# Kernel tuning notes

Measured on AMD Instinct MI355X. Metric: run time of the kernel, lower is better.

## Reference

```python
import jax, jax.numpy as jnp
import numpy as np

IN_F = 135; D = 512; K = 10; DCT_N = 34; IN_N = 120; OUT_N = 24
VL = K + OUT_N          # 34, window length
VN = IN_N - K - OUT_N + 1  # 87, number of windows
NSTAGE = 2
BN_SCALE = 1.0 / np.sqrt(1.0 + 1e-5)  # eval-mode BN with default running stats (mean 0, var 1)


def get_dct_matrix(N):
    dct_m = np.eye(N)
    for k in range(N):
        for i in range(N):
            w = np.sqrt(2.0 / N)
            if k == 0:
                w = np.sqrt(1.0 / N)
            dct_m[k, i] = w * np.cos(np.pi * (i + 0.5) * k / N)
    idct_m = np.linalg.inv(dct_m)
    return dct_m, idct_m

_DCT_NP, _IDCT_NP = get_dct_matrix(VL)
DCT = jnp.asarray(_DCT_NP[:DCT_N], dtype=jnp.float32)        # [34,34] (dct_n == vl)
IDCT = jnp.asarray(_IDCT_NP[:, :DCT_N], dtype=jnp.float32)   # [34,34]

WIN_IDX = np.arange(VL)[None, :] + np.arange(VN)[:, None]    # [87,34]
PAD_IDX = np.concatenate([np.arange(IN_N - K, IN_N), np.full(OUT_N, IN_N - 1)])  # last 10 frames + last frame repeated


def conv1d(x, w):
    return jax.lax.conv_general_dilated(x, w, (1,), 'VALID',
                                        dimension_numbers=('NCH', 'OIH', 'NCH'))


def gconv(x, att, w, b):
    # GraphConvolution: att @ (x @ w) + b ; x: [b,n,f_in]
    return jnp.einsum('nm,bmf->bnf', att, x @ w) + b


def bn_eval(y, g, b):
    bs, n, f = y.shape
    v = y.reshape(bs, n * f)
    v = g * (v * BN_SCALE) + b
    return v.reshape(bs, n, f)


def setup_inputs() -> dict:
    key = jax.random.key(0)
    ks = jax.random.split(key, 20)
    s = 0.05  # small init scale so tanh/att stay in sane range
    return {
        'poses':    jax.random.normal(ks[0], (256, 144, 135), jnp.float32),
        'qw1':      jax.random.normal(ks[1], (512, 135, 6)) * s,
        'qw2':      jax.random.normal(ks[2], (512, 512, 5)) * s,
        'kw1':      jax.random.normal(ks[3], (512, 135, 6)) * s,
        'kw2':      jax.random.normal(ks[4], (512, 512, 5)) * s,
        'gc1_att':  jax.random.normal(ks[5], (135, 135)) * s,
        'gc1_w':    jax.random.normal(ks[6], (68, 512)) * s,
        'gc1_b':    jax.random.normal(ks[7], (512,)) * s,
        'bn1_g':    jnp.ones((69120,), jnp.float32),
        'bn1_b':    jnp.zeros((69120,), jnp.float32),
        'gcb_att':  jax.random.normal(ks[8], (4, 135, 135)) * s,
        'gcb_w':    jax.random.normal(ks[9], (4, 512, 512)) * s,
        'gcb_b':    jax.random.normal(ks[10], (4, 512)) * s,
        'gcb_g':    jnp.ones((4, 69120), jnp.float32),
        'gcb_beta': jnp.zeros((4, 69120), jnp.float32),
        'gc7_att':  jax.random.normal(ks[11], (135, 135)) * s,
        'gc7_w':    jax.random.normal(ks[12], (512, 68)) * s,
        'gc7_b':    jax.random.normal(ks[13], (68,)) * s,
    }


def reference(poses, qw1, qw2, kw1, kw2,
              gc1_att, gc1_w, gc1_b, bn1_g, bn1_b,
              gcb_att, gcb_w, gcb_b, gcb_g, gcb_beta,
              gc7_att, gc7_w, gc7_b):
    src = poses[:, :IN_N]                      # [b,120,135]
    bs = src.shape[0]
    src_t = jnp.transpose(src, (0, 2, 1))      # [b,135,120]
    key_in = src_t[:, :, :IN_N - OUT_N] / 1000.0   # [b,135,96]
    qry_in = src_t[:, :, -K:] / 1000.0             # [b,135,10]

    key_f = jax.nn.relu(conv1d(jax.nn.relu(conv1d(key_in, kw1)), kw2))  # [b,512,87]
    qry_f = jax.nn.relu(conv1d(jax.nn.relu(conv1d(qry_in, qw1)), qw2))  # [b,512,1]

    # non-softmax attention: matmul + eps-normalize
    score = jnp.einsum('bdq,bdk->bqk', qry_f, key_f) + 1e-15   # [b,1,87]
    att = score / jnp.sum(score, axis=2, keepdims=True)

    # overlapping windows -> DCT of each window
    windows = src[:, WIN_IDX]                                   # [b,87,34,135]
    val = jnp.einsum('kt,bvtf->bvfk', DCT, windows).reshape(bs, VN, IN_F * DCT_N)
    dct_att = jnp.einsum('bqv,bvz->bqz', att, val)[:, 0].reshape(bs, IN_F, DCT_N)

    input_gcn = src[:, PAD_IDX]                                 # [b,34,135]
    dct_in = jnp.einsum('kt,btf->bfk', DCT, input_gcn)          # [b,135,34]
    x = jnp.concatenate([dct_in, dct_att], axis=-1)             # [b,135,68]

    # GCN (eval mode: dropout = identity, BN uses running stats)
    y = jnp.tanh(bn_eval(gconv(x, gc1_att, gc1_w, gc1_b), bn1_g, bn1_b))
    for i in range(NSTAGE):
        res = y
        h = jnp.tanh(bn_eval(gconv(y, gcb_att[2 * i], gcb_w[2 * i], gcb_b[2 * i]),
                             gcb_g[2 * i], gcb_beta[2 * i]))
        h = jnp.tanh(bn_eval(gconv(h, gcb_att[2 * i + 1], gcb_w[2 * i + 1], gcb_b[2 * i + 1]),
                             gcb_g[2 * i + 1], gcb_beta[2 * i + 1]))
        y = h + res
    y = gconv(y, gc7_att, gc7_w, gc7_b) + x                     # [b,135,68]

    out = jnp.einsum('tk,bfk->btf', IDCT, y[:, :, :DCT_N])      # [b,34,135]
    preds = out[:, -OUT_N:, :]                                  # [b,24,135]
    return preds
```

## Files before the change

kernel.cpp:

```cpp
#include <hip/hip_runtime.h>
#include <math.h>

#define POSE_ROWS 144
#define NF 135
#define DD 512
#define KQ 10
#define DCTN 34
#define INN 120
#define OUTN 24
#define VN 87
#define BATCH 256
#define RP 34816
#define NODEP 136
#define BN_SCALE 0.9999950000374997f

typedef __attribute__((ext_vector_type(8))) short short8;
typedef __attribute__((ext_vector_type(4))) float floatx4;

static __device__ __forceinline__ ushort f2bf(float f) {
    unsigned u = __builtin_bit_cast(unsigned, f);
    u = (u + 0x7FFFu + ((u >> 16) & 1u)) >> 16;
    return (ushort)u;
}
static __device__ __forceinline__ float bf2f(ushort s) {
    return __builtin_bit_cast(float, (unsigned)s << 16);
}
static __device__ __forceinline__ float tanh_fast(float x) {
    float ax = __builtin_fabsf(x);
    float e = __builtin_amdgcn_exp2f(ax * -2.885390081777927f);
    float t = (1.f - e) * __builtin_amdgcn_rcpf(1.f + e);
    return __builtin_copysignf(t, x);
}

#define GLOAD_LDS(gp, lp) __builtin_amdgcn_global_load_lds( \
    (const __attribute__((address_space(1))) unsigned int*)(const void*)(gp), \
    (__attribute__((address_space(3))) unsigned int*)(void*)(lp), 16, 0, 0)

#define PB_POSES 19584
#define PB_K1B   22912
#define PB_K2B   33152
#define PB_WT1   33408
#define PB_WTB   37504
#define PB_WT7   37640
#define PB_A1    37742
#define PB_AB    38147
#define PB_A7    38249
#define PB_BN    39609
#define PB_Z     39610
#define PB_DCT   39615

__global__ __launch_bounds__(256) void prep_all(
    const float* __restrict__ poses, ushort* __restrict__ pb16,
    const float* __restrict__ kw1, const float* __restrict__ qw1,
    ushort* __restrict__ Wt1k, ushort* __restrict__ Wt1q,
    const float* __restrict__ kw2, const float* __restrict__ qw2,
    ushort* __restrict__ Wt2k, ushort* __restrict__ Wt2q,
    const float* __restrict__ gc1_w, ushort* __restrict__ WT1,
    const float* __restrict__ gcb_w, ushort* __restrict__ WTb,
    const float* __restrict__ gc7_w, ushort* __restrict__ WT7,
    const float* __restrict__ gc1_att, ushort* __restrict__ A16_1,
    const float* __restrict__ gcb_att, ushort* __restrict__ A16_B,
    const float* __restrict__ gc7_att, ushort* __restrict__ A16_7,
    const float* __restrict__ bn1_g, const float* __restrict__ bn1_b,
    const float* __restrict__ gcb_g, const float* __restrict__ gcb_beta,
    float* __restrict__ bnT, float* __restrict__ zpadf, float* __restrict__ dct)
{
    const int blk = blockIdx.x;
    const int tid = threadIdx.x;
    if (blk < PB_POSES) {
        int idx = blk * 256 + tid;
        int i = idx % NODEP;
        int row = (idx / NODEP) % POSE_ROWS;
        int b = idx / (NODEP * POSE_ROWS);
        float v = (i < NF) ? poses[((long long)b * POSE_ROWS + row) * NF + i] * 1e-3f : 0.f;
        pb16[idx] = f2bf(v);
    } else if (blk < PB_K1B) {
        int wi = blk - PB_POSES;
        const float* src = (wi < 1664) ? kw1 : qw1;
        ushort* dst = (wi < 1664) ? Wt1k : Wt1q;
        int idx = (wi % 1664) * 256 + tid;
        int n = idx / 832, k = idx % 832;
        int h = k / 136, i = k % 136;
        float v = (i < 135 && h < 6) ? src[((long long)n * 135 + i) * 6 + h] : 0.f;
        dst[idx] = f2bf(v);
    } else if (blk < PB_K2B) {
        int wi = blk - PB_K1B;
        const float* src = (wi < 5120) ? kw2 : qw2;
        ushort* dst = (wi < 5120) ? Wt2k : Wt2q;
        int idx = (wi % 5120) * 256 + tid;
        int n = idx / 2560, k = idx % 2560;
        int h = k / 512, i = k % 512;
        dst[idx] = f2bf(src[((long long)n * 512 + i) * 5 + h]);
    } else if (blk < PB_WT1) {
        int idx = (blk - PB_K2B) * 256 + tid;
        int n = idx / 128, k = idx % 128;
        WT1[idx] = f2bf((k < 68) ? gc1_w[(long long)k * 512 + n] : 0.f);
    } else if (blk < PB_WTB) {
        int g = (blk - PB_WT1) * 256 + tid;
        int L = g >> 18, idx = g & 262143;
        int n = idx / 512, k = idx % 512;
        WTb[g] = f2bf(gcb_w[(long long)L * 262144 + (long long)k * 512 + n]);
    } else if (blk < PB_WT7) {
        int idx = (blk - PB_WTB) * 256 + tid;
        int n = idx / 512, k = idx % 512;
        WT7[idx] = f2bf(gc7_w[(long long)k * 68 + n]);
    } else if (blk < PB_A1) {
        int idx = (blk - PB_WT7) * 256 + tid;
        if (idx < 135 * 192) {
            int r = idx / 192, c = idx % 192;
            A16_1[idx] = f2bf(c < 135 ? gc1_att[r * 135 + c] : 0.f);
        }
    } else if (blk < PB_AB) {
        int idx = (blk - PB_A1) * 256 + tid;
        int r = idx / 192, c = idx % 192;
        A16_B[idx] = f2bf(c < 135 ? gcb_att[r * 135 + c] : 0.f);
    } else if (blk < PB_A7) {
        int idx = (blk - PB_AB) * 256 + tid;
        if (idx < 135 * 192) {
            int r = idx / 192, c = idx % 192;
            A16_7[idx] = f2bf(c < 135 ? gc7_att[r * 135 + c] : 0.f);
        }
    } else if (blk < PB_BN) {
        int g = (blk - PB_A7) * 256 + tid;
        int p = g / 69632, idx = g % 69632;
        int node = idx % 136, m = idx / 136;
        const float* gs = (p == 0) ? bn1_g : (gcb_g + (p - 1) * 69120);
        const float* bs = (p == 0) ? bn1_b : (gcb_beta + (p - 1) * 69120);
        float* gt = bnT + (long long)p * 139264;
        float* bt = gt + 69632;
        gt[idx] = (node < 135) ? gs[node * 512 + m] : 0.f;
        bt[idx] = (node < 135) ? bs[node * 512 + m] : 0.f;
    } else if (blk < PB_Z) {
        if (tid < 128) zpadf[tid] = 0.f;
    } else {
        int idx = (blk - PB_Z) * 256 + tid;
        if (idx < DCTN * DCTN) {
            int k = idx / DCTN, i = idx % DCTN;
            double w = (k == 0) ? sqrt(1.0 / DCTN) : sqrt(2.0 / DCTN);
            dct[idx] = (float)(w * cos(3.14159265358979323846 * (i + 0.5) * k / (double)DCTN));
        }
    }
}

template<int BM, int BN>
__global__ __launch_bounds__(256) void gemm2(
    const ushort* __restrict__ A, const ushort* __restrict__ Bt,
    const ushort* __restrict__ zpad,
    int M, int N, int K,
    int mode, int CNT, int Pc,
    int rpbA, long long sAw, long long sAr, long long sAbz,
    long long sBr, long long sBbz,
    float* __restrict__ C, ushort* __restrict__ C16,
    long long sCbz, long long sCm, long long sCn,
    int do_relu, const float* __restrict__ bias, int bias_mode,
    const float* __restrict__ bnTg, const float* __restrict__ bnTb,
    int do_tanh, const ushort* __restrict__ resid16, const float* __restrict__ resid32)
{
    constexpr int SM = BM / 32, SN = BN / 32;
    constexpr int RA = BM / 32, RB = BN / 32;
    __shared__ ushort As[BM * 64];
    __shared__ ushort Bs[BN * 64];

    int mb, nb;
    if (mode == 0) { mb = blockIdx.y; nb = blockIdx.x; }
    else {
        int gx = blockIdx.x;
        int x = gx & 7, s = gx >> 3;
        if (mode == 1) { mb = s % CNT; nb = x * Pc + s / CNT; }
        else           { nb = s % CNT; mb = x * Pc + s / CNT; }
    }
    const int m0 = mb * BM, n0 = nb * BN;
    if (m0 >= M || n0 >= N) return;

    const int tid = threadIdx.x;
    const int lane = tid & 63, w = tid >> 6;
    const int bz = blockIdx.z;
    const int wm = (w >> 1) * (BM / 2), wn = (w & 1) * (BN / 2);
    const int chunk = (lane & 7) ^ ((lane >> 3) & 7);

    const ushort* pA[RA]; int stA[RA];
    #pragma unroll
    for (int j = 0; j < RA; j++) {
        int m = m0 + j * 32 + w * 8 + (lane >> 3);
        bool v = m < M;
        long long off = v ? ((long long)(m / rpbA) * sAw + (long long)(m % rpbA) * sAr
                            + (long long)bz * sAbz) : 0;
        pA[j] = v ? (A + off + chunk * 8) : (zpad + chunk * 8);
        stA[j] = v ? 64 : 0;
    }
    const ushort* pB[RB]; int stB[RB];
    #pragma unroll
    for (int j = 0; j < RB; j++) {
        int n = n0 + j * 32 + w * 8 + (lane >> 3);
        bool v = n < N;
        long long off = v ? ((long long)n * sBr + (long long)bz * sBbz) : 0;
        pB[j] = v ? (Bt + off + chunk * 8) : (zpad + chunk * 8);
        stB[j] = v ? 64 : 0;
    }

    floatx4 acc[SM][SN];
    #pragma unroll
    for (int i = 0; i < SM; i++)
        #pragma unroll
        for (int j = 0; j < SN; j++)
            acc[i][j] = (floatx4){0.f, 0.f, 0.f, 0.f};

    for (int k0 = 0; k0 < K; k0 += 64) {
        #pragma unroll
        for (int j = 0; j < RA; j++)
            GLOAD_LDS(pA[j], &As[(j * 32 + w * 8) * 64]);
        #pragma unroll
        for (int j = 0; j < RB; j++)
            GLOAD_LDS(pB[j], &Bs[(j * 32 + w * 8) * 64]);
        __syncthreads();

        #pragma unroll
        for (int kk = 0; kk < 2; kk++) {
            short8 af[SM], bf[SN];
            #pragma unroll
            for (int sm = 0; sm < SM; sm++) {
                int lr = wm + sm * 16 + (lane & 15);
                int slot = ((lane >> 4) + kk * 4) ^ (lr & 7);
                af[sm] = *(const short8*)&As[lr * 64 + slot * 8];
            }
            #pragma unroll
            for (int sn = 0; sn < SN; sn++) {
                int lr = wn + sn * 16 + (lane & 15);
                int slot = ((lane >> 4) + kk * 4) ^ (lr & 7);
                bf[sn] = *(const short8*)&Bs[lr * 64 + slot * 8];
            }
            #pragma unroll
            for (int sm = 0; sm < SM; sm++)
                #pragma unroll
                for (int sn = 0; sn < SN; sn++)
                    acc[sm][sn] = __builtin_amdgcn_mfma_f32_16x16x32_bf16(af[sm], bf[sn], acc[sm][sn], 0, 0, 0);
        }
        __syncthreads();

        #pragma unroll
        for (int j = 0; j < RA; j++) pA[j] += stA[j];
        #pragma unroll
        for (int j = 0; j < RB; j++) pB[j] += stB[j];
    }

    const int lc = lane & 15;
    const int lr4 = (lane >> 4) << 2;
    #pragma unroll
    for (int sm = 0; sm < SM; sm++) {
        #pragma unroll
        for (int sn = 0; sn < SN; sn++) {
            int n = n0 + wn + sn * 16 + lc;
            if (n >= N) continue;
            int node = n % 136;
            int mbv = m0 + wm + sm * 16 + lr4;
            float vv[4];
            #pragma unroll
            for (int r = 0; r < 4; r++) {
                int m = mbv + r;
                float v = acc[sm][sn][r];
                if (do_relu) v = fmaxf(v, 0.f);
                if (bias) v += (bias_mode == 1) ? bias[m < M ? m : 0] : bias[n];
                if (bnTg) {
                    long long gi = (long long)(m < M ? m : 0) * 136 + node;
                    v = bnTg[gi] * (v * BN_SCALE) + bnTb[gi];
                }
                if (do_tanh) v = tanh_fast(v);
                long long addr = (long long)bz * sCbz + (long long)m * sCm + (long long)n * sCn;
                if (m < M) {
                    if (resid16) v += bf2f(resid16[addr]);
                    else if (resid32) v += resid32[addr];
                    if (C) C[addr] = v;
                    if (C16 && sCm != 1) C16[addr] = f2bf(v);
                }
                vv[r] = v;
            }
            if (C16 && sCm == 1 && mbv + 3 < M) {
                ushort4 pk;
                pk.x = f2bf(vv[0]); pk.y = f2bf(vv[1]); pk.z = f2bf(vv[2]); pk.w = f2bf(vv[3]);
                *(ushort4*)&C16[(long long)bz * sCbz + mbv + (long long)n * sCn] = pk;
            }
        }
    }
}

__global__ __launch_bounds__(512) void fused_layer(
    const ushort* __restrict__ Yin,
    const ushort* __restrict__ Att,
    const ushort* __restrict__ Wt,
    const ushort* __restrict__ zpad,
    const float* __restrict__ bias,
    const float* __restrict__ bnTg, const float* __restrict__ bnTb,
    const ushort* __restrict__ resid16,
    ushort* __restrict__ Yout)
{
    extern __shared__ ushort zs[];
    const int b = blockIdx.x;
    const int tid = threadIdx.x;
    const int lane = tid & 63, w = tid >> 6;
    const int ln = lane & 15;
    const int lk8 = (lane >> 4) * 8;
    const int lr4 = (lane >> 4) << 2;
    const long long ybase = (long long)b * 136;
    const int cp = w * 64;

    {
        const ushort* pb[9];
        #pragma unroll
        for (int nt = 0; nt < 9; nt++) {
            int n = nt * 16 + ln;
            pb[nt] = (n < 135) ? (Att + (long long)n * 192 + lk8) : (zpad + lk8);
        }
        const ushort* pa[4];
        #pragma unroll
        for (int sm = 0; sm < 4; sm++) {
            int c = cp + sm * 16 + ln;
            pa[sm] = Yin + (long long)c * RP + ybase + lk8;
        }
        floatx4 acc[4][9];
        #pragma unroll
        for (int i = 0; i < 4; i++)
            #pragma unroll
            for (int j = 0; j < 9; j++)
                acc[i][j] = (floatx4){0.f, 0.f, 0.f, 0.f};

        #pragma unroll
        for (int ks = 0; ks < 5; ks++) {
            const int ko = ks * 32;
            short8 af[4];
            #pragma unroll
            for (int sm = 0; sm < 4; sm++)
                af[sm] = *(const short8*)(pa[sm] + ko);
            #pragma unroll
            for (int nt = 0; nt < 9; nt++) {
                short8 bfv = *(const short8*)(pb[nt] + ko);
                #pragma unroll
                for (int sm = 0; sm < 4; sm++)
                    acc[sm][nt] = __builtin_amdgcn_mfma_f32_16x16x32_bf16(af[sm], bfv, acc[sm][nt], 0, 0, 0);
            }
        }
        #pragma unroll
        for (int sm = 0; sm < 4; sm++) {
            #pragma unroll
            for (int nt = 0; nt < 9; nt++) {
                int n = nt * 16 + ln;
                if (n >= 136) continue;
                int c = cp + sm * 16 + lr4;
                ushort4 pk;
                pk.x = f2bf(acc[sm][nt][0]);
                pk.y = f2bf(acc[sm][nt][1]);
                pk.z = f2bf(acc[sm][nt][2]);
                pk.w = f2bf(acc[sm][nt][3]);
                int chs = (c >> 3) ^ (n & 7);
                *(ushort4*)&zs[n * 512 + chs * 8 + (c & 7)] = pk;
            }
        }
    }
    __syncthreads();

    {
        const ushort* pw[4];
        #pragma unroll
        for (int sm = 0; sm < 4; sm++)
            pw[sm] = Wt + (long long)(cp + sm * 16 + ln) * 512 + lk8;
        int zrow[9], zx[9];
        #pragma unroll
        for (int nt = 0; nt < 9; nt++) {
            int n = nt * 16 + ln;
            int nn = (n < 136) ? n : 0;
            zrow[nt] = nn * 512;
            zx[nt] = nn & 7;
        }
        floatx4 acc[4][9];
        #pragma unroll
        for (int i = 0; i < 4; i++)
            #pragma unroll
            for (int j = 0; j < 9; j++)
                acc[i][j] = (floatx4){0.f, 0.f, 0.f, 0.f};

        #pragma unroll
        for (int ks = 0; ks < 16; ks++) {
            const int ko = ks * 32;
            const int kchunk = ks * 4 + (lane >> 4);
            short8 af[4];
            #pragma unroll
            for (int sm = 0; sm < 4; sm++)
                af[sm] = *(const short8*)(pw[sm] + ko);
            #pragma unroll
            for (int nt = 0; nt < 9; nt++) {
                short8 bfv = *(const short8*)&zs[zrow[nt] + (kchunk ^ zx[nt]) * 8];
                #pragma unroll
                for (int sm = 0; sm < 4; sm++)
                    acc[sm][nt] = __builtin_amdgcn_mfma_f32_16x16x32_bf16(af[sm], bfv, acc[sm][nt], 0, 0, 0);
            }
        }
        #pragma unroll
        for (int sm = 0; sm < 4; sm++) {
            #pragma unroll
            for (int nt = 0; nt < 9; nt++) {
                int n = nt * 16 + ln;
                if (n >= 136) continue;
                int c2 = cp + sm * 16 + lr4;
                #pragma unroll
                for (int r = 0; r < 4; r++) {
                    int m = c2 + r;
                    float v = acc[sm][nt][r];
                    v += bias[m];
                    long long gi = (long long)m * 136 + n;
                    v = bnTg[gi] * (v * BN_SCALE) + bnTb[gi];
                    v = tanh_fast(v);
                    long long addr = (long long)m * RP + ybase + n;
                    if (resid16) v += bf2f(resid16[addr]);
                    Yout[addr] = f2bf(v);
                }
            }
        }
    }
}

__global__ __launch_bounds__(256) void att_k(const float* __restrict__ kf, const float* __restrict__ qf,
                                             float* __restrict__ att) {
    int b = blockIdx.x;
    int tid = threadIdx.x;
    int lane = tid & 63, w = tid >> 6;
    __shared__ float s[96];
    __shared__ float ssum;
    const float* qb = qf + b * DD + lane * 8;
    float4 q0 = *(const float4*)qb;
    float4 q1 = *(const float4*)(qb + 4);
    const float* kb = kf + (long long)b * VN * DD;
    for (int v = w; v < VN; v += 4) {
        const float* kr = kb + v * DD + lane * 8;
        float4 k0 = *(const float4*)kr;
        float4 k1 = *(const float4*)(kr + 4);
        float p = q0.x * k0.x + q0.y * k0.y + q0.z * k0.z + q0.w * k0.w
                + q1.x * k1.x + q1.y * k1.y + q1.z * k1.z + q1.w * k1.w;
        #pragma unroll
        for (int off = 32; off; off >>= 1) p += __shfl_xor(p, off);
        if (lane == 0) s[v] = p + 1e-15f;
    }
    __syncthreads();
    if (tid < 64) {
        float p2 = (tid < VN ? s[tid] : 0.f) + ((tid + 64) < VN ? s[tid + 64] : 0.f);
        #pragma unroll
        for (int off = 32; off; off >>= 1) p2 += __shfl_xor(p2, off);
        if (tid == 0) ssum = p2;
    }
    __syncthreads();
    float inv = 1.f / ssum;
    for (int v = tid; v < VN; v += 256) att[b * VN + v] = s[v] * inv;
}

__global__ void weighted_k(const float* __restrict__ poses, const float* __restrict__ att,
                           float* __restrict__ w34) {
    int t = blockIdx.x;
    int b = blockIdx.y;
    int f = threadIdx.x;
    if (f >= NF) return;
    const float* pb = poses + (long long)b * POSE_ROWS * NF + t * NF + f;
    const float* ab = att + b * VN;
    float acc = 0.f;
    for (int v = 0; v < VN; v++) acc += ab[v] * pb[v * NF];
    w34[(long long)b * DCTN * NF + t * NF + f] = acc;
}

__global__ void build_x(const float* __restrict__ poses, const float* __restrict__ w34,
                        const float* __restrict__ dctm, float* __restrict__ x32,
                        ushort* __restrict__ xT16) {
    int idx = blockIdx.x * 256 + threadIdx.x;
    if (idx >= BATCH * NF * 68) return;
    int kk = idx % 68;
    int f = (idx / 68) % NF;
    int b = idx / (68 * NF);
    float acc = 0.f;
    if (kk < DCTN) {
        const float* pb = poses + (long long)b * POSE_ROWS * NF;
        #pragma unroll
        for (int t = 0; t < DCTN; t++) {
            int row = (t < KQ) ? (INN - KQ + t) : (INN - 1);
            acc += dctm[kk * DCTN + t] * pb[row * NF + f];
        }
    } else {
        int k2 = kk - DCTN;
        const float* wb = w34 + (long long)b * DCTN * NF + f;
        #pragma unroll
        for (int t = 0; t < DCTN; t++) acc += dctm[k2 * DCTN + t] * wb[t * NF];
    }
    long long R = (long long)b * NODEP + f;
    x32[R * 68 + kk] = acc;
    xT16[(long long)kk * RP + R] = f2bf(acc);
}

__global__ void idct_out(const float* __restrict__ h32, const float* __restrict__ dctm,
                         float* __restrict__ out) {
    int idx = blockIdx.x * 256 + threadIdx.x;
    if (idx >= BATCH * OUTN * NF) return;
    int f = idx % NF;
    int t = (idx / NF) % OUTN;
    int b = idx / (NF * OUTN);
    const float* yr = h32 + ((long long)b * NODEP + f) * 68;
    float acc = 0.f;
    #pragma unroll
    for (int k = 0; k < DCTN; k++) acc += dctm[k * DCTN + (KQ + t)] * yr[k];
    out[idx] = acc;
}

extern "C" void kernel_launch(void* const* d_in, const int* in_sizes, int n_in,
                              void* d_out, int out_size, void* d_ws, size_t ws_size,
                              hipStream_t stream) {
    const float* poses   = (const float*)d_in[0];
    const float* qw1     = (const float*)d_in[1];
    const float* qw2     = (const float*)d_in[2];
    const float* kw1     = (const float*)d_in[3];
    const float* kw2     = (const float*)d_in[4];
    const float* gc1_att = (const float*)d_in[5];
    const float* gc1_w   = (const float*)d_in[6];
    const float* gc1_b   = (const float*)d_in[7];
    const float* bn1_g   = (const float*)d_in[8];
    const float* bn1_b   = (const float*)d_in[9];
    const float* gcb_att = (const float*)d_in[10];
    const float* gcb_w   = (const float*)d_in[11];
    const float* gcb_b   = (const float*)d_in[12];
    const float* gcb_g   = (const float*)d_in[13];
    const float* gcb_beta= (const float*)d_in[14];
    const float* gc7_att = (const float*)d_in[15];
    const float* gc7_w   = (const float*)d_in[16];
    const float* gc7_b   = (const float*)d_in[17];
    float* out = (float*)d_out;
    float* w = (float*)d_ws;

    float* dct   = w;
    float* att   = w + 1280;
    float* w34   = w + 23808;
    float* x32   = w + 1198848;
    float* h32   = w + 3566336;
    float* qf    = w + 5933824;
    ushort* su   = (ushort*)(w + 6064896);
    ushort* WT1    = su;
    ushort* WTb    = su + 65536;
    ushort* WT7    = su + 1114112;
    ushort* A16_1  = su + 1148928;
    ushort* A16_B  = su + 1174848;
    ushort* A16_7  = su + 1278528;
    float* bnT   = w + 6717120;
    float* kf    = w + 7413440;
    ushort* R2   = (ushort*)(w + 18816704);
    ushort* yT16  = R2;
    ushort* r1k16 = R2;
    ushort* r1q16 = R2 + 11927552;
    ushort* R3   = (ushort*)(w + 27729600);
    ushort* hT16  = R3;
    ushort* pb16  = R3;
    ushort* Wt1k  = R3 + 5013504;
    ushort* Wt1q  = R3 + 5439488;
    ushort* Wt2k  = R3 + 5865472;
    ushort* Wt2q  = R3 + 7176192;
    ushort* R4   = (ushort*)(w + 36642496);
    ushort* zN16  = R4;
    ushort* xT16  = R4;
    ushort* z116  = R4 + 2367488;
    float* zpadf = w + 45555392;
    const ushort* zpad = (const ushort*)zpadf;

    const int INF_RPB = 1 << 30;

    static int lds_set = 0;
    if (!lds_set) {
        hipFuncSetAttribute((const void*)fused_layer,
                            hipFuncAttributeMaxDynamicSharedMemorySize, 139264);
        lds_set = 1;
    }

    prep_all<<<PB_DCT, 256, 0, stream>>>(
        poses, pb16, kw1, qw1, Wt1k, Wt1q, kw2, qw2, Wt2k, Wt2q,
        gc1_w, WT1, gcb_w, WTb, gc7_w, WT7,
        gc1_att, A16_1, gcb_att, A16_B, gc7_att, A16_7,
        bn1_g, bn1_b, gcb_g, gcb_beta, bnT, zpadf, dct);

    gemm2<128,64><<<dim3(1472, 1, 1), 256, 0, stream>>>(pb16, Wt1k, zpad, 23296, 512, 832,
        2, 8, 23, 91, 19584LL, 136LL, 0LL, 832LL, 0LL,
        (float*)nullptr, r1k16, 0LL, 512LL, 1LL, 1, nullptr, 0, nullptr, nullptr, 0, nullptr, nullptr);
    gemm2<128,128><<<dim3(4, 10, 1), 256, 0, stream>>>(pb16 + 110*136, Wt1q, zpad, 1280, 512, 832,
        0, 0, 0, 5, 19584LL, 136LL, 0LL, 832LL, 0LL,
        (float*)nullptr, r1q16, 0LL, 512LL, 1LL, 1, nullptr, 0, nullptr, nullptr, 0, nullptr, nullptr);
    gemm2<128,64><<<dim3(1408, 1, 1), 256, 0, stream>>>(r1k16, Wt2k, zpad, 22272, 512, 2560,
        2, 8, 22, 87, 46592LL, 512LL, 0LL, 2560LL, 0LL,
        kf, (ushort*)nullptr, 0LL, 512LL, 1LL, 1, nullptr, 0, nullptr, nullptr, 0, nullptr, nullptr);
    gemm2<64,64><<<dim3(8, 4, 1), 256, 0, stream>>>(r1q16, Wt2q, zpad, 256, 512, 2560,
        0, 0, 0, INF_RPB, 0LL, 2560LL, 0LL, 2560LL, 0LL,
        qf, (ushort*)nullptr, 0LL, 512LL, 1LL, 1, nullptr, 0, nullptr, nullptr, 0, nullptr, nullptr);

    att_k<<<BATCH, 256, 0, stream>>>(kf, qf, att);
    weighted_k<<<dim3(DCTN, BATCH), 192, 0, stream>>>(poses, att, w34);
    build_x<<<(BATCH * NF * 68 + 255) / 256, 256, 0, stream>>>(poses, w34, dct, x32, xT16);

    gemm2<64,64><<<dim3(3, 2, BATCH), 256, 0, stream>>>(xT16, A16_1, zpad, 68, 135, 192,
        0, 0, 0, INF_RPB, 0LL, (long long)RP, 136LL, 192LL, 0LL,
        (float*)nullptr, z116, 10880LL, 1LL, 80LL, 0, nullptr, 0, nullptr, nullptr, 0, nullptr, nullptr);
    gemm2<128,64><<<dim3(2176, 1, 1), 256, 0, stream>>>(WT1, z116, zpad, 512, RP, 128,
        1, 4, 68, INF_RPB, 0LL, 128LL, 0LL, 80LL, 0LL,
        (float*)nullptr, yT16, 0LL, (long long)RP, 1LL, 0, gc1_b, 1, bnT, bnT + 69632, 1, nullptr, nullptr);

    for (int L = 0; L < 4; L++) {
        const ushort* min = (L & 1) ? hT16 : yT16;
        ushort* mout = (L & 1) ? yT16 : hT16;
        fused_layer<<<dim3(BATCH, 1, 1), 512, 139264, stream>>>(
            min, A16_B + L * 25920, WTb + L * 262144, zpad,
            gcb_b + L * 512, bnT + (1 + L) * 139264, bnT + (1 + L) * 139264 + 69632,
            (L & 1) ? yT16 : (const ushort*)nullptr, mout);
    }

    gemm2<64,64><<<dim3(3, 8, BATCH), 256, 0, stream>>>(yT16, A16_7, zpad, 512, 135, 192,
        0, 0, 0, INF_RPB, 0LL, (long long)RP, 136LL, 192LL, 0LL,
        (float*)nullptr, zN16, 69632LL, 1LL, 512LL, 0, nullptr, 0, nullptr, nullptr, 0, nullptr, nullptr);
    gemm2<64,64><<<dim3(1088, 1, 1), 256, 0, stream>>>(zN16, WT7, zpad, RP, 68, 512,
        2, 2, 68, INF_RPB, 0LL, 512LL, 0LL, 512LL, 0LL,
        h32, (ushort*)nullptr, 0LL, 68LL, 1LL, 0, gc7_b, 2, nullptr, nullptr, 0, nullptr, x32);

    idct_out<<<(BATCH * OUTN * NF + 255) / 256, 256, 0, stream>>>(h32, dct, out);
}
```

Measured before the change: 895.7 us.

## Store GCN activations batch-major so each sample's features are contiguous

Changes the activation layout yT16/hT16 from channel-major with batch interleaved (stride RP per channel) to batch-major (BSTRIDE per sample, 136 per channel). The gc1 epilogue gets a bmaj addressing mode, and fused_layer and the gc7 att GEMM are updated to index the new layout. The intent is for each fused_layer block to read and write one contiguous 139 KB slab instead of 512 strided rows spread across the whole tensor, which should improve cache and DRAM locality. In exchange, the gc1 epilogue's stores are now scattered by n/136, which may coalesce less well.

```diff
diff --git a/kernel.cpp b/kernel.cpp
--- a/kernel.cpp
+++ b/kernel.cpp
@@ -12,6 +12,7 @@
 #define BATCH 256
 #define RP 34816
 #define NODEP 136
+#define BSTRIDE 69632
 #define BN_SCALE 0.9999950000374997f
 
 typedef __attribute__((ext_vector_type(8))) short short8;
@@ -154,7 +155,8 @@
     long long sCbz, long long sCm, long long sCn,
     int do_relu, const float* __restrict__ bias, int bias_mode,
     const float* __restrict__ bnTg, const float* __restrict__ bnTb,
-    int do_tanh, const ushort* __restrict__ resid16, const float* __restrict__ resid32)
+    int do_tanh, const ushort* __restrict__ resid16, const float* __restrict__ resid32,
+    int bmaj)
 {
     constexpr int SM = BM / 32, SN = BN / 32;
     constexpr int RA = BM / 32, RB = BN / 32;
@@ -265,7 +267,9 @@
                     v = bnTg[gi] * (v * BN_SCALE) + bnTb[gi];
                 }
                 if (do_tanh) v = tanh_fast(v);
-                long long addr = (long long)bz * sCbz + (long long)m * sCm + (long long)n * sCn;
+                long long addr = bmaj
+                    ? (long long)(n / 136) * BSTRIDE + (long long)m * 136 + node
+                    : (long long)bz * sCbz + (long long)m * sCm + (long long)n * sCn;
                 if (m < M) {
                     if (resid16) v += bf2f(resid16[addr]);
                     else if (resid32) v += resid32[addr];
@@ -300,7 +304,7 @@
     const int ln = lane & 15;
     const int lk8 = (lane >> 4) * 8;
     const int lr4 = (lane >> 4) << 2;
-    const long long ybase = (long long)b * 136;
+    const long long ybase = (long long)b * BSTRIDE;
     const int cp = w * 64;
 
     {
@@ -314,7 +318,7 @@
         #pragma unroll
         for (int sm = 0; sm < 4; sm++) {
             int c = cp + sm * 16 + ln;
-            pa[sm] = Yin + (long long)c * RP + ybase + lk8;
+            pa[sm] = Yin + ybase + (long long)c * 136 + lk8;
         }
         floatx4 acc[4][9];
         #pragma unroll
@@ -408,7 +412,7 @@
                     long long gi = (long long)m * 136 + n;
                     v = bnTg[gi] * (v * BN_SCALE) + bnTb[gi];
                     v = tanh_fast(v);
-                    long long addr = (long long)m * RP + ybase + n;
+                    long long addr = ybase + (long long)m * 136 + n;
                     if (resid16) v += bf2f(resid16[addr]);
                     Yout[addr] = f2bf(v);
                 }
@@ -578,16 +582,16 @@
 
     gemm2<128,64><<<dim3(1472, 1, 1), 256, 0, stream>>>(pb16, Wt1k, zpad, 23296, 512, 832,
         2, 8, 23, 91, 19584LL, 136LL, 0LL, 832LL, 0LL,
-        (float*)nullptr, r1k16, 0LL, 512LL, 1LL, 1, nullptr, 0, nullptr, nullptr, 0, nullptr, nullptr);
+        (float*)nullptr, r1k16, 0LL, 512LL, 1LL, 1, nullptr, 0, nullptr, nullptr, 0, nullptr, nullptr, 0);
     gemm2<128,128><<<dim3(4, 10, 1), 256, 0, stream>>>(pb16 + 110*136, Wt1q, zpad, 1280, 512, 832,
         0, 0, 0, 5, 19584LL, 136LL, 0LL, 832LL, 0LL,
-        (float*)nullptr, r1q16, 0LL, 512LL, 1LL, 1, nullptr, 0, nullptr, nullptr, 0, nullptr, nullptr);
+        (float*)nullptr, r1q16, 0LL, 512LL, 1LL, 1, nullptr, 0, nullptr, nullptr, 0, nullptr, nullptr, 0);
     gemm2<128,64><<<dim3(1408, 1, 1), 256, 0, stream>>>(r1k16, Wt2k, zpad, 22272, 512, 2560,
         2, 8, 22, 87, 46592LL, 512LL, 0LL, 2560LL, 0LL,
-        kf, (ushort*)nullptr, 0LL, 512LL, 1LL, 1, nullptr, 0, nullptr, nullptr, 0, nullptr, nullptr);
+        kf, (ushort*)nullptr, 0LL, 512LL, 1LL, 1, nullptr, 0, nullptr, nullptr, 0, nullptr, nullptr, 0);
     gemm2<64,64><<<dim3(8, 4, 1), 256, 0, stream>>>(r1q16, Wt2q, zpad, 256, 512, 2560,
         0, 0, 0, INF_RPB, 0LL, 2560LL, 0LL, 2560LL, 0LL,
-        qf, (ushort*)nullptr, 0LL, 512LL, 1LL, 1, nullptr, 0, nullptr, nullptr, 0, nullptr, nullptr);
+        qf, (ushort*)nullptr, 0LL, 512LL, 1LL, 1, nullptr, 0, nullptr, nullptr, 0, nullptr, nullptr, 0);
 
     att_k<<<BATCH, 256, 0, stream>>>(kf, qf, att);
     weighted_k<<<dim3(DCTN, BATCH), 192, 0, stream>>>(poses, att, w34);
@@ -595,10 +599,10 @@
 
     gemm2<64,64><<<dim3(3, 2, BATCH), 256, 0, stream>>>(xT16, A16_1, zpad, 68, 135, 192,
         0, 0, 0, INF_RPB, 0LL, (long long)RP, 136LL, 192LL, 0LL,
-        (float*)nullptr, z116, 10880LL, 1LL, 80LL, 0, nullptr, 0, nullptr, nullptr, 0, nullptr, nullptr);
+        (float*)nullptr, z116, 10880LL, 1LL, 80LL, 0, nullptr, 0, nullptr, nullptr, 0, nullptr, nullptr, 0);
     gemm2<128,64><<<dim3(2176, 1, 1), 256, 0, stream>>>(WT1, z116, zpad, 512, RP, 128,
         1, 4, 68, INF_RPB, 0LL, 128LL, 0LL, 80LL, 0LL,
-        (float*)nullptr, yT16, 0LL, (long long)RP, 1LL, 0, gc1_b, 1, bnT, bnT + 69632, 1, nullptr, nullptr);
+        (float*)nullptr, yT16, 0LL, (long long)RP, 1LL, 0, gc1_b, 1, bnT, bnT + 69632, 1, nullptr, nullptr, 1);
 
     for (int L = 0; L < 4; L++) {
         const ushort* min = (L & 1) ? hT16 : yT16;
@@ -610,11 +614,11 @@
     }
 
     gemm2<64,64><<<dim3(3, 8, BATCH), 256, 0, stream>>>(yT16, A16_7, zpad, 512, 135, 192,
-        0, 0, 0, INF_RPB, 0LL, (long long)RP, 136LL, 192LL, 0LL,
-        (float*)nullptr, zN16, 69632LL, 1LL, 512LL, 0, nullptr, 0, nullptr, nullptr, 0, nullptr, nullptr);
+        0, 0, 0, INF_RPB, 0LL, 136LL, (long long)BSTRIDE, 192LL, 0LL,
+        (float*)nullptr, zN16, 69632LL, 1LL, 512LL, 0, nullptr, 0, nullptr, nullptr, 0, nullptr, nullptr, 0);
     gemm2<64,64><<<dim3(1088, 1, 1), 256, 0, stream>>>(zN16, WT7, zpad, RP, 68, 512,
         2, 2, 68, INF_RPB, 0LL, 512LL, 0LL, 512LL, 0LL,
-        h32, (ushort*)nullptr, 0LL, 68LL, 1LL, 0, gc7_b, 2, nullptr, nullptr, 0, nullptr, x32);
+        h32, (ushort*)nullptr, 0LL, 68LL, 1LL, 0, gc7_b, 2, nullptr, nullptr, 0, nullptr, x32, 0);
 
     idct_out<<<(BATCH * OUTN * NF + 255) / 256, 256, 0, stream>>>(h32, dct, out);
 }
```

Result: no change. 896.4 us (+0.1%).
